# Performance work log

Hardware: AMD Instinct MI355X
Metric: run time of the kernel (lower is better)

Reference implementation:

```python
import jax, jax.numpy as jnp
import numpy as np

N_ROUTINGS = 3
EPS = 1e-9


def squash(s):
    # s: [..., dim_capsule]
    norm_sq = jnp.sum(s * s, axis=-1, keepdims=True)
    scale = norm_sq / (1.0 + norm_sq) / jnp.sqrt(norm_sq + EPS)
    return scale * s


def setup_inputs() -> dict:
    key = jax.random.key(0)
    k1, k2 = jax.random.split(key, 2)
    batch, n_in, d_in = 32, 2048, 16
    n_cap, d_cap = 64, 32
    x = jax.random.normal(k1, (batch, n_in, d_in), dtype=jnp.float32)
    # glorot-uniform-ish init for W
    limit = np.sqrt(6.0 / (d_in + d_cap)).astype(np.float32)
    W = jax.random.uniform(k2, (n_in, n_cap, d_in, d_cap), dtype=jnp.float32,
                           minval=-limit, maxval=limit)
    B = jnp.zeros((n_cap, d_cap), dtype=jnp.float32)
    return {"x": x, "W": W, "B": B}


def reference(x, W, B):
    # x: [b, n, d_in], W: [n, c, d_in, e], B: [c, e]
    # predictions u: [b, n, c, e]  (equivalent to the tiled matmul in TF)
    u = jnp.einsum('bnd,ncde->bnce', x, W) + B[None, None, :, :]
    b = jnp.zeros(u.shape[:3], dtype=u.dtype)  # [b, n, c]
    v = None
    for _ in range(N_ROUTINGS):
        c = jax.nn.softmax(b, axis=-1)                 # [b, n, c]
        s = jnp.einsum('bnce,bnc->bce', u, c)          # [b, c, e]
        v = squash(s)                                  # [b, c, e]
        b = b + jnp.einsum('bnce,bce->bnc', u, v)      # agreement update
    return v
```

## Files before the change

### kernel.cpp

```cpp
#include <hip/hip_runtime.h>
#include <hip/hip_bf16.h>

typedef unsigned int uint32;

#define BATCH 32
#define NIN   2048
#define DIN   16
#define NCAP  64
#define DCAP  32
#define ROW   2048

__device__ __forceinline__ uint32 pack_bf2(float a, float b){
    union { __hip_bfloat16 h; ushort u; } ca, cb;
    ca.h = __float2bfloat16(a);
    cb.h = __float2bfloat16(b);
    return (uint32)ca.u | ((uint32)cb.u << 16);
}
__device__ __forceinline__ float bf_lo(uint32 w){ return __uint_as_float(w << 16); }
__device__ __forceinline__ float bf_hi(uint32 w){ return __uint_as_float(w & 0xffff0000u); }

__global__ __launch_bounds__(256, 2)
void k1_predict(const float* __restrict__ x, const float* __restrict__ W,
                const float* __restrict__ Bc, __hip_bfloat16* __restrict__ u,
                ushort* __restrict__ part)
{
    __shared__ float xs[8 * 32 * 16];
    const int t     = threadIdx.x;
    const int half  = blockIdx.x;
    const int chunk = blockIdx.y;
    const int n0    = chunk * 8;
    const int cl    = t >> 3;
    const int e0    = (t & 7) * 4;
    const int cg    = half * 32 + cl;

    #pragma unroll
    for (int k = 0; k < 4; ++k) {
        const int f = (t + 256 * k) * 4;
        const int i = f >> 9, rem = f & 511, b = rem >> 4, d = rem & 15;
        *(float4*)(xs + f) = *(const float4*)(x + ((size_t)b * NIN + n0 + i) * DIN + d);
    }
    __syncthreads();

    const float4 bias = *(const float4*)(Bc + cg * DCAP + e0);

    float sacc[32][4];
    #pragma unroll
    for (int b = 0; b < 32; ++b) {
        sacc[b][0] = 0.f; sacc[b][1] = 0.f; sacc[b][2] = 0.f; sacc[b][3] = 0.f;
    }

    const float* wbase = W + (size_t)cg * (DIN * DCAP) + e0;
    for (int i = 0; i < 8; ++i) {
        const int n = n0 + i;
        float4 w[16];
        {
            const float* wp = wbase + (size_t)n * (NCAP * DIN * DCAP);
            #pragma unroll
            for (int d = 0; d < 16; ++d) w[d] = *(const float4*)(wp + d * DCAP);
        }
        const float* xrow = xs + i * 512;
        __hip_bfloat16* ub = u + (size_t)n * ROW + cg * DCAP + e0;

        #pragma unroll
        for (int b = 0; b < 32; ++b) {
            float4 uv = bias;
            #pragma unroll
            for (int d4 = 0; d4 < 4; ++d4) {
                const float4 xv = *(const float4*)(xrow + b * 16 + d4 * 4);
                uv.x = fmaf(xv.x, w[d4*4+0].x, uv.x);
                uv.y = fmaf(xv.x, w[d4*4+0].y, uv.y);
                uv.z = fmaf(xv.x, w[d4*4+0].z, uv.z);
                uv.w = fmaf(xv.x, w[d4*4+0].w, uv.w);
                uv.x = fmaf(xv.y, w[d4*4+1].x, uv.x);
                uv.y = fmaf(xv.y, w[d4*4+1].y, uv.y);
                uv.z = fmaf(xv.y, w[d4*4+1].z, uv.z);
                uv.w = fmaf(xv.y, w[d4*4+1].w, uv.w);
                uv.x = fmaf(xv.z, w[d4*4+2].x, uv.x);
                uv.y = fmaf(xv.z, w[d4*4+2].y, uv.y);
                uv.z = fmaf(xv.z, w[d4*4+2].z, uv.z);
                uv.w = fmaf(xv.z, w[d4*4+2].w, uv.w);
                uv.x = fmaf(xv.w, w[d4*4+3].x, uv.x);
                uv.y = fmaf(xv.w, w[d4*4+3].y, uv.y);
                uv.z = fmaf(xv.w, w[d4*4+3].z, uv.z);
                uv.w = fmaf(xv.w, w[d4*4+3].w, uv.w);
            }
            sacc[b][0] += uv.x; sacc[b][1] += uv.y;
            sacc[b][2] += uv.z; sacc[b][3] += uv.w;
            uint2 pk;
            pk.x = pack_bf2(uv.x, uv.y);
            pk.y = pack_bf2(uv.z, uv.w);
            *(uint2*)(ub + (size_t)b * (NIN * ROW)) = pk;
        }
    }

    #pragma unroll
    for (int b = 0; b < 32; ++b) {
        uint2 pk;
        pk.x = pack_bf2(sacc[b][0], sacc[b][1]);
        pk.y = pack_bf2(sacc[b][2], sacc[b][3]);
        *(uint2*)(part + ((size_t)b * 256 + chunk) * ROW + cg * DCAP + e0) = pk;
    }
}

__global__ __launch_bounds__(64)
void k2_squash(const void* __restrict__ partv, int nch, int isbf16, float factor,
               float* __restrict__ V, float* __restrict__ out, int first)
{
    const int t  = threadIdx.x;
    const int b  = blockIdx.y;
    const int p0 = (blockIdx.x * 64 + t) * 4;

    float a0 = 0.f, a1 = 0.f, a2 = 0.f, a3 = 0.f;
    if (isbf16) {
        const ushort* pp = (const ushort*)partv;
        #pragma unroll 4
        for (int ch = 0; ch < nch; ++ch) {
            const uint2 v = *(const uint2*)(pp + ((size_t)b * nch + ch) * ROW + p0);
            a0 += bf_lo(v.x); a1 += bf_hi(v.x);
            a2 += bf_lo(v.y); a3 += bf_hi(v.y);
        }
    } else {
        const float* pp = (const float*)partv;
        #pragma unroll 4
        for (int ch = 0; ch < nch; ++ch) {
            const float4 v = *(const float4*)(pp + ((size_t)b * nch + ch) * ROW + p0);
            a0 += v.x; a1 += v.y; a2 += v.z; a3 += v.w;
        }
    }
    a0 *= factor; a1 *= factor; a2 *= factor; a3 *= factor;

    float nsq = a0*a0 + a1*a1 + a2*a2 + a3*a3;
    nsq += __shfl_xor(nsq, 1);
    nsq += __shfl_xor(nsq, 2);
    nsq += __shfl_xor(nsq, 4);
    const float scale = nsq / ((1.f + nsq) * sqrtf(nsq + 1e-9f));
    const float v0 = scale*a0, v1 = scale*a1, v2 = scale*a2, v3 = scale*a3;

    const size_t idx = (size_t)b * ROW + p0;
    float4 Vn;
    if (first) Vn = make_float4(v0, v1, v2, v3);
    else {
        const float4 old = *(const float4*)(V + idx);
        Vn = make_float4(old.x+v0, old.y+v1, old.z+v2, old.w+v3);
    }
    *(float4*)(V + idx) = Vn;
    if (out) *(float4*)(out + idx) = make_float4(v0, v1, v2, v3);
}

__global__ __launch_bounds__(256)
void k3_sweep(const __hip_bfloat16* __restrict__ u, const float* __restrict__ V,
              float* __restrict__ part)
{
    __shared__ float red[4 * 2112];
    const int t     = threadIdx.x;
    const int lane  = t & 63;
    const int wv    = t >> 6;
    const int chunk = blockIdx.x;
    const int b     = blockIdx.y;

    const int qr = lane >> 2;
    const int es = (lane & 3) * 8;

    float vr[4][8];
    #pragma unroll
    for (int q = 0; q < 4; ++q) {
        const float* vp = V + (size_t)b * ROW + (q * 16 + qr) * DCAP + es;
        const float4 v0 = *(const float4*)(vp);
        const float4 v1 = *(const float4*)(vp + 4);
        vr[q][0]=v0.x; vr[q][1]=v0.y; vr[q][2]=v0.z; vr[q][3]=v0.w;
        vr[q][4]=v1.x; vr[q][5]=v1.y; vr[q][6]=v1.z; vr[q][7]=v1.w;
    }

    float sacc[4][8];
    #pragma unroll
    for (int q = 0; q < 4; ++q)
        #pragma unroll
        for (int j = 0; j < 8; ++j) sacc[q][j] = 0.f;

    const int nbase = chunk * 64 + wv * 16;
    const __hip_bfloat16* ubase = u + ((size_t)b * NIN + nbase) * ROW + lane * 8;

    uint4 A[4];
    #pragma unroll
    for (int q = 0; q < 4; ++q)
        A[q] = *(const uint4*)(ubase + q * 512);

    for (int it = 0; it < 16; ++it) {
        uint4 Bn[4];
        if (it < 15) {
            const __hip_bfloat16* un = ubase + (size_t)(it + 1) * ROW;
            #pragma unroll
            for (int q = 0; q < 4; ++q)
                Bn[q] = *(const uint4*)(un + q * 512);
        }

        float p[4];
        #pragma unroll
        for (int q = 0; q < 4; ++q) {
            const uint32 w0 = A[q].x, w1 = A[q].y, w2 = A[q].z, w3 = A[q].w;
            float l0 = bf_lo(w0) * vr[q][0];
            float l1 = bf_hi(w0) * vr[q][1];
            l0 = fmaf(bf_lo(w1), vr[q][2], l0);
            l1 = fmaf(bf_hi(w1), vr[q][3], l1);
            l0 = fmaf(bf_lo(w2), vr[q][4], l0);
            l1 = fmaf(bf_hi(w2), vr[q][5], l1);
            l0 = fmaf(bf_lo(w3), vr[q][6], l0);
            l1 = fmaf(bf_hi(w3), vr[q][7], l1);
            p[q] = l0 + l1;
        }
        #pragma unroll
        for (int q = 0; q < 4; ++q) {
            p[q] += __shfl_xor(p[q], 1);
            p[q] += __shfl_xor(p[q], 2);
        }
        float e0 = __expf(p[0]), e1 = __expf(p[1]),
              e2 = __expf(p[2]), e3 = __expf(p[3]);
        float s = (e0 + e1) + (e2 + e3);
        s += __shfl_xor(s, 4);
        s += __shfl_xor(s, 8);
        s += __shfl_xor(s, 16);
        s += __shfl_xor(s, 32);
        const float inv = 4.0f / s;
        const float cw[4] = {e0 * inv, e1 * inv, e2 * inv, e3 * inv};

        #pragma unroll
        for (int q = 0; q < 4; ++q) {
            const uint32 w0 = A[q].x, w1 = A[q].y, w2 = A[q].z, w3 = A[q].w;
            const float c = cw[q];
            sacc[q][0] = fmaf(c, bf_lo(w0), sacc[q][0]);
            sacc[q][1] = fmaf(c, bf_hi(w0), sacc[q][1]);
            sacc[q][2] = fmaf(c, bf_lo(w1), sacc[q][2]);
            sacc[q][3] = fmaf(c, bf_hi(w1), sacc[q][3]);
            sacc[q][4] = fmaf(c, bf_lo(w2), sacc[q][4]);
            sacc[q][5] = fmaf(c, bf_hi(w2), sacc[q][5]);
            sacc[q][6] = fmaf(c, bf_lo(w3), sacc[q][6]);
            sacc[q][7] = fmaf(c, bf_hi(w3), sacc[q][7]);
        }

        if (it < 15) {
            #pragma unroll
            for (int q = 0; q < 4; ++q) A[q] = Bn[q];
        }
    }

    #pragma unroll
    for (int q = 0; q < 4; ++q) {
        const int c = q * 16 + qr;
        #pragma unroll
        for (int j = 0; j < 8; ++j)
            red[wv * 2112 + c * 33 + es + j] = sacc[q][j];
    }
    __syncthreads();
    #pragma unroll
    for (int k = 0; k < 8; ++k) {
        const int pp = t + 256 * k;
        const int c = pp >> 5, e = pp & 31;
        part[((size_t)b * 32 + chunk) * ROW + pp] =
            red[0*2112 + c*33+e] + red[1*2112 + c*33+e] +
            red[2*2112 + c*33+e] + red[3*2112 + c*33+e];
    }
}

extern "C" void kernel_launch(void* const* d_in, const int* in_sizes, int n_in,
                              void* d_out, int out_size, void* d_ws, size_t ws_size,
                              hipStream_t stream)
{
    const float* x  = (const float*)d_in[0];
    const float* W  = (const float*)d_in[1];
    const float* Bc = (const float*)d_in[2];
    float* out = (float*)d_out;

    const size_t off_u    = 0;
    const size_t off_part = 268435456;
    const size_t off_V    = off_part + 33554432;
    const size_t need     = off_V + 262144;
    if (ws_size < need) return;

    __hip_bfloat16* u  = (__hip_bfloat16*)((char*)d_ws + off_u);
    ushort* part_bf    = (ushort*)((char*)d_ws + off_part);
    float*  part_f     = (float*)((char*)d_ws + off_part);
    float*  V          = (float*)((char*)d_ws + off_V);

    k1_predict<<<dim3(2, 256), 256, 0, stream>>>(x, W, Bc, u, part_bf);
    k2_squash <<<dim3(8, BATCH), 64, 0, stream>>>(part_bf, 256, 1, 1.0f/64.0f, V, nullptr, 1);
    k3_sweep  <<<dim3(32, BATCH), 256, 0, stream>>>(u, V, part_f);
    k2_squash <<<dim3(8, BATCH), 64, 0, stream>>>(part_f, 32, 0, 1.0f, V, nullptr, 0);
    k3_sweep  <<<dim3(32, BATCH), 256, 0, stream>>>(u, V, part_f);
    k2_squash <<<dim3(8, BATCH), 64, 0, stream>>>(part_f, 32, 0, 1.0f, V, out, 0);
}
```

Measured before the change: 263.3 us.

## Split k1 batch dimension across thread groups to raise parallelism and cut registers

```diff
diff --git a/kernel.cpp b/kernel.cpp
--- a/kernel.cpp
+++ b/kernel.cpp
@@ -19,19 +19,21 @@
 __device__ __forceinline__ float bf_lo(uint32 w){ return __uint_as_float(w << 16); }
 __device__ __forceinline__ float bf_hi(uint32 w){ return __uint_as_float(w & 0xffff0000u); }
 
-__global__ __launch_bounds__(256, 2)
+__global__ __launch_bounds__(256)
 void k1_predict(const float* __restrict__ x, const float* __restrict__ W,
                 const float* __restrict__ Bc, __hip_bfloat16* __restrict__ u,
                 ushort* __restrict__ part)
 {
     __shared__ float xs[8 * 32 * 16];
     const int t     = threadIdx.x;
-    const int half  = blockIdx.x;
+    const int capg  = blockIdx.x;
     const int chunk = blockIdx.y;
     const int n0    = chunk * 8;
-    const int cl    = t >> 3;
+    const int bg    = t >> 6;
+    const int cl    = (t >> 3) & 7;
     const int e0    = (t & 7) * 4;
-    const int cg    = half * 32 + cl;
+    const int cg    = capg * 8 + cl;
+    const int b0    = bg * 8;
 
     #pragma unroll
     for (int k = 0; k < 4; ++k) {
@@ -43,10 +45,10 @@
 
     const float4 bias = *(const float4*)(Bc + cg * DCAP + e0);
 
-    float sacc[32][4];
-    #pragma unroll
-    for (int b = 0; b < 32; ++b) {
-        sacc[b][0] = 0.f; sacc[b][1] = 0.f; sacc[b][2] = 0.f; sacc[b][3] = 0.f;
+    float sacc[8][4];
+    #pragma unroll
+    for (int bi = 0; bi < 8; ++bi) {
+        sacc[bi][0] = 0.f; sacc[bi][1] = 0.f; sacc[bi][2] = 0.f; sacc[bi][3] = 0.f;
     }
 
     const float* wbase = W + (size_t)cg * (DIN * DCAP) + e0;
@@ -58,15 +60,15 @@
             #pragma unroll
             for (int d = 0; d < 16; ++d) w[d] = *(const float4*)(wp + d * DCAP);
         }
-        const float* xrow = xs + i * 512;
-        __hip_bfloat16* ub = u + (size_t)n * ROW + cg * DCAP + e0;
-
-        #pragma unroll
-        for (int b = 0; b < 32; ++b) {
+        const float* xrow = xs + i * 512 + b0 * 16;
+        __hip_bfloat16* ub = u + ((size_t)b0 * NIN + n) * ROW + cg * DCAP + e0;
+
+        #pragma unroll
+        for (int bi = 0; bi < 8; ++bi) {
             float4 uv = bias;
             #pragma unroll
             for (int d4 = 0; d4 < 4; ++d4) {
-                const float4 xv = *(const float4*)(xrow + b * 16 + d4 * 4);
+                const float4 xv = *(const float4*)(xrow + bi * 16 + d4 * 4);
                 uv.x = fmaf(xv.x, w[d4*4+0].x, uv.x);
                 uv.y = fmaf(xv.x, w[d4*4+0].y, uv.y);
                 uv.z = fmaf(xv.x, w[d4*4+0].z, uv.z);
@@ -84,21 +86,21 @@
                 uv.z = fmaf(xv.w, w[d4*4+3].z, uv.z);
                 uv.w = fmaf(xv.w, w[d4*4+3].w, uv.w);
             }
-            sacc[b][0] += uv.x; sacc[b][1] += uv.y;
-            sacc[b][2] += uv.z; sacc[b][3] += uv.w;
+            sacc[bi][0] += uv.x; sacc[bi][1] += uv.y;
+            sacc[bi][2] += uv.z; sacc[bi][3] += uv.w;
             uint2 pk;
             pk.x = pack_bf2(uv.x, uv.y);
             pk.y = pack_bf2(uv.z, uv.w);
-            *(uint2*)(ub + (size_t)b * (NIN * ROW)) = pk;
-        }
-    }
-
-    #pragma unroll
-    for (int b = 0; b < 32; ++b) {
+            *(uint2*)(ub + (size_t)bi * (NIN * ROW)) = pk;
+        }
+    }
+
+    #pragma unroll
+    for (int bi = 0; bi < 8; ++bi) {
         uint2 pk;
-        pk.x = pack_bf2(sacc[b][0], sacc[b][1]);
-        pk.y = pack_bf2(sacc[b][2], sacc[b][3]);
-        *(uint2*)(part + ((size_t)b * 256 + chunk) * ROW + cg * DCAP + e0) = pk;
+        pk.x = pack_bf2(sacc[bi][0], sacc[bi][1]);
+        pk.y = pack_bf2(sacc[bi][2], sacc[bi][3]);
+        *(uint2*)(part + ((size_t)(b0 + bi) * 256 + chunk) * ROW + cg * DCAP + e0) = pk;
     }
 }
 
@@ -281,7 +283,7 @@
     float*  part_f     = (float*)((char*)d_ws + off_part);
     float*  V          = (float*)((char*)d_ws + off_V);
 
-    k1_predict<<<dim3(2, 256), 256, 0, stream>>>(x, W, Bc, u, part_bf);
+    k1_predict<<<dim3(8, 256), 256, 0, stream>>>(x, W, Bc, u, part_bf);
     k2_squash <<<dim3(8, BATCH), 64, 0, stream>>>(part_bf, 256, 1, 1.0f/64.0f, V, nullptr, 1);
     k3_sweep  <<<dim3(32, BATCH), 256, 0, stream>>>(u, V, part_f);
     k2_squash <<<dim3(8, BATCH), 64, 0, stream>>>(part_f, 32, 0, 1.0f, V, nullptr, 0);
```

Measured after the change: 423.6 us. 1.61x slower.

## Use hardware bf16 pack, bf16 partial accumulators, drop x LDS staging

Applied to the files above, without the earlier changes.

```diff
diff --git a/kernel.cpp b/kernel.cpp
--- a/kernel.cpp
+++ b/kernel.cpp
@@ -10,21 +10,19 @@
 #define DCAP  32
 #define ROW   2048
 
-__device__ __forceinline__ uint32 pack_bf2(float a, float b){
-    union { __hip_bfloat16 h; ushort u; } ca, cb;
-    ca.h = __float2bfloat16(a);
-    cb.h = __float2bfloat16(b);
-    return (uint32)ca.u | ((uint32)cb.u << 16);
+__device__ __forceinline__ uint32 cvt_pk_bf16(float lo, float hi){
+    uint32 r;
+    asm("v_cvt_pk_bf16_f32 %0, %1, %2" : "=v"(r) : "v"(lo), "v"(hi));
+    return r;
 }
 __device__ __forceinline__ float bf_lo(uint32 w){ return __uint_as_float(w << 16); }
 __device__ __forceinline__ float bf_hi(uint32 w){ return __uint_as_float(w & 0xffff0000u); }
 
-__global__ __launch_bounds__(256, 2)
+__global__ __launch_bounds__(256)
 void k1_predict(const float* __restrict__ x, const float* __restrict__ W,
                 const float* __restrict__ Bc, __hip_bfloat16* __restrict__ u,
                 ushort* __restrict__ part)
 {
-    __shared__ float xs[8 * 32 * 16];
     const int t     = threadIdx.x;
     const int half  = blockIdx.x;
     const int chunk = blockIdx.y;
@@ -33,23 +31,14 @@
     const int e0    = (t & 7) * 4;
     const int cg    = half * 32 + cl;
 
-    #pragma unroll
-    for (int k = 0; k < 4; ++k) {
-        const int f = (t + 256 * k) * 4;
-        const int i = f >> 9, rem = f & 511, b = rem >> 4, d = rem & 15;
-        *(float4*)(xs + f) = *(const float4*)(x + ((size_t)b * NIN + n0 + i) * DIN + d);
-    }
-    __syncthreads();
-
     const float4 bias = *(const float4*)(Bc + cg * DCAP + e0);
 
-    float sacc[32][4];
-    #pragma unroll
-    for (int b = 0; b < 32; ++b) {
-        sacc[b][0] = 0.f; sacc[b][1] = 0.f; sacc[b][2] = 0.f; sacc[b][3] = 0.f;
-    }
+    uint32 spk[32][2];
+    #pragma unroll
+    for (int b = 0; b < 32; ++b) { spk[b][0] = 0u; spk[b][1] = 0u; }
 
     const float* wbase = W + (size_t)cg * (DIN * DCAP) + e0;
+
     for (int i = 0; i < 8; ++i) {
         const int n = n0 + i;
         float4 w[16];
@@ -58,15 +47,16 @@
             #pragma unroll
             for (int d = 0; d < 16; ++d) w[d] = *(const float4*)(wp + d * DCAP);
         }
-        const float* xrow = xs + i * 512;
         __hip_bfloat16* ub = u + (size_t)n * ROW + cg * DCAP + e0;
-
-        #pragma unroll
-        for (int b = 0; b < 32; ++b) {
+        const float* xrow = x + (size_t)n * DIN;
+
+        #pragma unroll
+        for (int bi = 0; bi < 32; ++bi) {
+            const float* xr = xrow + (size_t)bi * (NIN * DIN);
             float4 uv = bias;
             #pragma unroll
             for (int d4 = 0; d4 < 4; ++d4) {
-                const float4 xv = *(const float4*)(xrow + b * 16 + d4 * 4);
+                const float4 xv = *(const float4*)(xr + d4 * 4);
                 uv.x = fmaf(xv.x, w[d4*4+0].x, uv.x);
                 uv.y = fmaf(xv.x, w[d4*4+0].y, uv.y);
                 uv.z = fmaf(xv.x, w[d4*4+0].z, uv.z);
@@ -84,20 +74,20 @@
                 uv.z = fmaf(xv.w, w[d4*4+3].z, uv.z);
                 uv.w = fmaf(xv.w, w[d4*4+3].w, uv.w);
             }
-            sacc[b][0] += uv.x; sacc[b][1] += uv.y;
-            sacc[b][2] += uv.z; sacc[b][3] += uv.w;
             uint2 pk;
-            pk.x = pack_bf2(uv.x, uv.y);
-            pk.y = pack_bf2(uv.z, uv.w);
-            *(uint2*)(ub + (size_t)b * (NIN * ROW)) = pk;
+            pk.x = cvt_pk_bf16(uv.x, uv.y);
+            pk.y = cvt_pk_bf16(uv.z, uv.w);
+            *(uint2*)(ub + (size_t)bi * (NIN * ROW)) = pk;
+            spk[bi][0] = cvt_pk_bf16(bf_lo(spk[bi][0]) + uv.x,
+                                     bf_hi(spk[bi][0]) + uv.y);
+            spk[bi][1] = cvt_pk_bf16(bf_lo(spk[bi][1]) + uv.z,
+                                     bf_hi(spk[bi][1]) + uv.w);
         }
     }
 
     #pragma unroll
     for (int b = 0; b < 32; ++b) {
-        uint2 pk;
-        pk.x = pack_bf2(sacc[b][0], sacc[b][1]);
-        pk.y = pack_bf2(sacc[b][2], sacc[b][3]);
+        uint2 pk; pk.x = spk[b][0]; pk.y = spk[b][1];
         *(uint2*)(part + ((size_t)b * 256 + chunk) * ROW + cg * DCAP + e0) = pk;
     }
 }
```

Result: slower. 335.9 us (+27.6%).
